# Optimization experiments

Measured on AMD Instinct MI355X. Metric: run time of the kernel, lower is better.

## Reference

```python
import jax, jax.numpy as jnp
import numpy as np

N = 50000      # nodes
E = 800000     # edges (avg degree 16)
G = 256        # graphs in batch
DIN = 126      # input feature dim (hardcoded in module)
H = 128        # dim_h


def _lin_init(key, fan_in, shape):
    s = 1.0 / np.sqrt(fan_in)
    return jax.random.uniform(key, shape, minval=-s, maxval=s, dtype=jnp.float32)


def setup_inputs() -> dict:
    key = jax.random.key(0)
    ks = iter(jax.random.split(key, 64))
    inp = {}
    inp["x"] = jax.random.normal(next(ks), (N, DIN), dtype=jnp.float32)
    inp["edge_attr"] = jax.random.normal(next(ks), (E, 4), dtype=jnp.float32)  # unused by the conv (edge_dim=None)
    dims = [(DIN, H), (H, H), (H, H)]
    for l, (i, o) in enumerate(dims, start=1):
        for nm, bnm in [("Wk", "bk"), ("Wq", "bq"), ("Wv", "bv"), ("Ws", "bs")]:
            inp[f"{nm}{l}"] = _lin_init(next(ks), i, (i, o))
            inp[f"{bnm}{l}"] = _lin_init(next(ks), i, (o,))
    inp["W4"] = _lin_init(next(ks), H, (H, 64))
    inp["b4"] = _lin_init(next(ks), H, (64,))
    inp["W5"] = _lin_init(next(ks), 64, (64, 1))
    inp["b5"] = _lin_init(next(ks), 64, (1,))
    inp["edge_index"] = jax.random.randint(next(ks), (2, E), 0, N, dtype=jnp.int64)
    inp["batch"] = jnp.sort(jax.random.randint(next(ks), (N,), 0, G, dtype=jnp.int64))
    return inp


def _res_gated_conv(x, src, dst, Wk, bk, Wq, bq, Wv, bv, Ws, bs):
    # PyG ResGatedGraphConv: out_i = skip(x_i) + sum_j sigmoid(K_i + Q_j) * V_j
    K = x @ Wk + bk   # [N, H] keys (destination / x_i)
    Q = x @ Wq + bq   # [N, H] queries (source / x_j)
    V = x @ Wv + bv   # [N, H] values (source / x_j)
    gate = jax.nn.sigmoid(K[dst] + Q[src])           # [E, H]
    msg = gate * V[src]                              # [E, H]
    agg = jax.ops.segment_sum(msg, dst, num_segments=x.shape[0])  # scatter-add to dst
    return agg + x @ Ws + bs  # lin_skip (no bias) + conv bias


def reference(x, edge_attr,
              Wk1, bk1, Wq1, bq1, Wv1, bv1, Ws1, bs1,
              Wk2, bk2, Wq2, bq2, Wv2, bv2, Ws2, bs2,
              Wk3, bk3, Wq3, bq3, Wv3, bv3, Ws3, bs3,
              W4, b4, W5, b5, edge_index, batch):
    src, dst = edge_index[0], edge_index[1]
    h = jax.nn.relu(_res_gated_conv(x, src, dst, Wk1, bk1, Wq1, bq1, Wv1, bv1, Ws1, bs1))
    h = jax.nn.relu(_res_gated_conv(h, src, dst, Wk2, bk2, Wq2, bq2, Wv2, bv2, Ws2, bs2))
    h = _res_gated_conv(h, src, dst, Wk3, bk3, Wq3, bq3, Wv3, bv3, Ws3, bs3)
    # global_add_pool over graphs
    hg = jax.ops.segment_sum(h, batch, num_segments=G)  # [G, H]
    hg = jax.nn.relu(hg @ W4 + b4)
    return jax.nn.sigmoid(hg @ W5 + b5)  # [G, 1]
```

## Files before the change

kernel.cpp:

```cpp
#include <hip/hip_runtime.h>

#define N_NODES 50000
#define N_EDGES 800000
#define N_GRAPHS 256
#define DIN 126
#define H 128
#define MP 50048
#define NBKT 196
#define NBA 100
#define CHA 8000

typedef __attribute__((ext_vector_type(8))) _Float16 half8v;
typedef __attribute__((ext_vector_type(4))) _Float16 half4v;
typedef __attribute__((ext_vector_type(4))) float f32x4;
typedef __attribute__((ext_vector_type(2))) float f32x2;

__global__ __launch_bounds__(256) void conv_A(const float* __restrict__ X, int M, int Kd,
                                              _Float16* __restrict__ A16)
{
    const int t = blockIdx.x * 256 + threadIdx.x;
    const int row = t >> 4;
    if (row >= MP) return;
    const int k0 = (t & 15) * 8;
    half8v v8;
    #pragma unroll
    for (int j = 0; j < 8; ++j) {
        const int k = k0 + j;
        float v = 0.f;
        if (row < M && k < Kd) v = X[(size_t)row * Kd + k];
        v8[j] = (_Float16)v;
    }
    *(half8v*)&A16[(size_t)row * 128 + k0] = v8;
}

struct WPtrs { const float* w[12]; };

__global__ __launch_bounds__(256) void conv_W3(WPtrs P, _Float16* __restrict__ Wt16)
{
    const int t = blockIdx.x * 256 + threadIdx.x;
    if (t >= 3 * 512 * 128) return;
    const int layer = t >> 16;
    const int r = t & 65535;
    const int n = r >> 7, k = r & 127;
    const int mtx = n >> 7, cc = n & 127;
    const int Kd = (layer == 0) ? DIN : H;
    const float* W = P.w[layer * 4 + mtx];
    const float v = (k < Kd) ? W[(size_t)k * 128 + cc] : 0.f;
    Wt16[t] = (_Float16)v;
}

__device__ __forceinline__ void dense_out512(const uint2 (&ldsO)[64][32],
                                             unsigned char* __restrict__ dst,
                                             int row0, int M, int t)
{
    #pragma unroll
    for (int i = 0; i < 2; ++i) {
        const int idx = i * 512 + t;
        const int rr = idx >> 4, c16 = idx & 15;
        const int ch = c16 ^ ((rr & 15) >> 1);
        const uint2 a = ldsO[rr][2 * ch];
        const uint2 b = ldsO[rr][2 * ch + 1];
        if (row0 + rr < M) {
            uint4 o;
            if (rr & 1) { o.x = b.x; o.y = b.y; o.z = a.x; o.w = a.y; }
            else        { o.x = a.x; o.y = a.y; o.z = b.x; o.w = b.y; }
            *(uint4*)(dst + (size_t)(row0 + rr) * 256 + c16 * 16) = o;
        }
    }
}

__device__ __forceinline__ void compute_acc16(const _Float16 (&ldsA)[2][64 * 64],
                                              const _Float16* __restrict__ Wt16,
                                              int mtx, int fr, int kq, int colbase,
                                              f32x4 (&acc)[4])
{
    #pragma unroll
    for (int step = 0; step < 4; ++step) {
        const int kg = step * 4 + kq;
        const int kh = kg >> 3, kk = kg & 7;
        half8v a[4];
        #pragma unroll
        for (int m = 0; m < 4; ++m) {
            const int ar = m * 16 + fr;
            const int slot = kk ^ (ar & 7);
            a[m] = *(const half8v*)&ldsA[kh][ar * 64 + slot * 8];
        }
        const size_t wo = (size_t)(mtx * 128 + colbase + fr) * 128 + kg * 8;
        const half8v w = *(const half8v*)&Wt16[wo];
        #pragma unroll
        for (int m = 0; m < 4; ++m)
            acc[m] = __builtin_amdgcn_mfma_f32_16x16x32_f16(w, a[m], acc[m], 0, 0, 0);
    }
}

__global__ __launch_bounds__(512) void gemm_mfma(
    const _Float16* __restrict__ A16, const _Float16* __restrict__ Wt16,
    const float* __restrict__ bias0, const float* __restrict__ bias1,
    const float* __restrict__ bias2, const float* __restrict__ bias3,
    _Float16* __restrict__ OEK, unsigned char* __restrict__ QV8,
    _Float16* __restrict__ OS, int M)
{
    __shared__ _Float16 ldsA[2][64 * 64];
    __shared__ uint2 ldsO[64][32];
    const int t = threadIdx.x;
    const int l = t & 63, w = t >> 6;
    const int row0 = blockIdx.x * 64;
    const int fr = l & 15;
    const int kq = l >> 4;
    const int colbase = w * 16;

    #pragma unroll
    for (int i = 0; i < 2; ++i) {
        const int gi = i * 512 + t;
        const int kh = gi >> 9;
        const int r = (gi >> 3) & 63;
        const int j = gi & 7;
        const int slot = j ^ (r & 7);
        *(half8v*)&ldsA[kh][r * 64 + slot * 8] =
            *(const half8v*)&A16[(size_t)(row0 + r) * 128 + kh * 64 + j * 8];
    }
    __syncthreads();

    const int c0 = colbase + kq * 4;
    const int qd = (c0 >> 2) ^ fr;

    {
        f32x4 acc[4] = {};
        compute_acc16(ldsA, Wt16, 0, fr, kq, colbase, acc);
        const float4 bv = *(const float4*)&bias0[c0];
        #pragma unroll
        for (int m = 0; m < 4; ++m) {
            const int rl = m * 16 + fr;
            half4v o;
            o[0] = (_Float16)__expf(-(acc[m][0] + bv.x));
            o[1] = (_Float16)__expf(-(acc[m][1] + bv.y));
            o[2] = (_Float16)__expf(-(acc[m][2] + bv.z));
            o[3] = (_Float16)__expf(-(acc[m][3] + bv.w));
            ldsO[rl][qd] = *(uint2*)&o;
        }
    }
    __syncthreads();
    dense_out512(ldsO, (unsigned char*)OEK, row0, M, t);
    __syncthreads();

    {
        f32x4 acc[4] = {};
        compute_acc16(ldsA, Wt16, 1, fr, kq, colbase, acc);
        const float4 bv = *(const float4*)&bias1[c0];
        #pragma unroll
        for (int m = 0; m < 4; ++m) {
            const int rl = m * 16 + fr;
            const float e0 = __expf(-(acc[m][0] + bv.x));
            const float e1 = __expf(-(acc[m][1] + bv.y));
            const float e2 = __expf(-(acc[m][2] + bv.z));
            const float e3 = __expf(-(acc[m][3] + bv.w));
            int p = 0;
            p = __builtin_amdgcn_cvt_pk_fp8_f32(e0, e1, p, false);
            p = __builtin_amdgcn_cvt_pk_fp8_f32(e2, e3, p, true);
            ((unsigned*)&ldsO[rl][qd])[0] = (unsigned)p;
        }
    }
    {
        f32x4 acc[4] = {};
        compute_acc16(ldsA, Wt16, 2, fr, kq, colbase, acc);
        const float4 bv = *(const float4*)&bias2[c0];
        #pragma unroll
        for (int m = 0; m < 4; ++m) {
            const int rl = m * 16 + fr;
            int p = 0;
            p = __builtin_amdgcn_cvt_pk_fp8_f32(acc[m][0] + bv.x,
                                                acc[m][1] + bv.y, p, false);
            p = __builtin_amdgcn_cvt_pk_fp8_f32(acc[m][2] + bv.z,
                                                acc[m][3] + bv.w, p, true);
            ((unsigned*)&ldsO[rl][qd])[1] = (unsigned)p;
        }
    }
    __syncthreads();
    dense_out512(ldsO, QV8, row0, M, t);
    __syncthreads();

    {
        f32x4 acc[4] = {};
        compute_acc16(ldsA, Wt16, 3, fr, kq, colbase, acc);
        const float4 bv = *(const float4*)&bias3[c0];
        #pragma unroll
        for (int m = 0; m < 4; ++m) {
            const int rl = m * 16 + fr;
            half4v o;
            o[0] = (_Float16)(acc[m][0] + bv.x);
            o[1] = (_Float16)(acc[m][1] + bv.y);
            o[2] = (_Float16)(acc[m][2] + bv.z);
            o[3] = (_Float16)(acc[m][3] + bv.w);
            ldsO[rl][qd] = *(uint2*)&o;
        }
    }
    __syncthreads();
    dense_out512(ldsO, (unsigned char*)OS, row0, M, t);
}

__global__ __launch_bounds__(256) void pA_hist(const int* __restrict__ ei,
                                               int* __restrict__ ghA)
{
    __shared__ int lh[NBKT];
    const int t = threadIdx.x, b = blockIdx.x;
    if (t < NBKT) lh[t] = 0;
    __syncthreads();
    const int e0 = b * CHA;
    for (int i = t; i < CHA; i += 256)
        atomicAdd(&lh[ei[N_EDGES + e0 + i] >> 8], 1);
    __syncthreads();
    if (t < NBKT) ghA[t * NBA + b] = lh[t];
}

__global__ __launch_bounds__(1024) void pA_scan(int* __restrict__ g)
{
    __shared__ int part[1024];
    const int t = threadIdx.x;
    const int NT = NBKT * NBA;
    const int CH = 20;
    const int base = t * CH;
    int s = 0;
    for (int i = 0; i < CH; ++i) {
        const int idx = base + i;
        if (idx < NT) s += g[idx];
    }
    part[t] = s;
    __syncthreads();
    for (int d = 1; d < 1024; d <<= 1) {
        const int v = (t >= d) ? part[t - d] : 0;
        __syncthreads();
        part[t] += v;
        __syncthreads();
    }
    int run = (t == 0) ? 0 : part[t - 1];
    for (int i = 0; i < CH; ++i) {
        const int idx = base + i;
        if (idx < NT) { const int c = g[idx]; g[idx] = run; run += c; }
    }
    if (t == 1023) g[NT] = part[1023];
}

__global__ __launch_bounds__(256) void pA_scat(const int* __restrict__ ei,
                                               const int* __restrict__ gbase,
                                               unsigned int* __restrict__ ebuf)
{
    __shared__ int cur[NBKT];
    const int t = threadIdx.x, b = blockIdx.x;
    if (t < NBKT) cur[t] = gbase[t * NBA + b];
    __syncthreads();
    const int e0 = b * CHA;
    for (int i = t; i < CHA; i += 256) {
        const unsigned d = (unsigned)ei[N_EDGES + e0 + i];
        const unsigned s = (unsigned)ei[e0 + i];
        const int pos = atomicAdd(&cur[d >> 8], 1);
        ebuf[pos] = (d << 16) | s;
    }
}

__global__ __launch_bounds__(256) void pB_build(const unsigned int* __restrict__ ebuf,
                                                const int* __restrict__ gbase,
                                                int* __restrict__ off,
                                                int* __restrict__ csr)
{
    __shared__ int lh[256], sc[256];
    const int t = threadIdx.x, b = blockIdx.x;
    const int beg = gbase[b * NBA];
    const int end = gbase[(b + 1) * NBA];
    lh[t] = 0;
    __syncthreads();
    for (int i = beg + t; i < end; i += 256)
        atomicAdd(&lh[(ebuf[i] >> 16) & 255], 1);
    __syncthreads();
    const int c = lh[t];
    sc[t] = c;
    __syncthreads();
    for (int d = 1; d < 256; d <<= 1) {
        const int v = (t >= d) ? sc[t - d] : 0;
        __syncthreads();
        sc[t] += v;
        __syncthreads();
    }
    const int excl = sc[t] - c;
    const int nd = b * 256 + t;
    if (nd <= N_NODES) off[nd] = beg + excl;
    __syncthreads();
    lh[t] = beg + excl;
    __syncthreads();
    for (int i = beg + t; i < end; i += 256) {
        const unsigned p = ebuf[i];
        const int pos = atomicAdd(&lh[(p >> 16) & 255], 1);
        csr[pos] = (int)(p & 0xFFFFu);
    }
}

template<int FUSE>
__global__ __launch_bounds__(256) void agg_csr(
    const _Float16* __restrict__ EKb, const unsigned char* __restrict__ QV8,
    const int* __restrict__ off, const int* __restrict__ csr_src,
    _Float16* __restrict__ hSkip, _Float16* __restrict__ A16, int Nn)
{
    const int node = blockIdx.x * 4 + (threadIdx.x >> 6);
    if (node >= Nn) return;
    const int lane = threadIdx.x & 63;
    const int grp = lane >> 4;
    const int sub = lane & 15;
    const int q = sub * 8;

    const half8v ek8 = *(const half8v*)(EKb + (size_t)node * H + q);
    float ek[8];
    #pragma unroll
    for (int i = 0; i < 8; ++i) ek[i] = (float)ek8[i];
    float acc[8] = {};

    const int begin = off[node], end = off[node + 1];
    for (int j0 = begin; j0 < end; j0 += 64) {
        const int nrem = end - j0;
        const int nk = nrem < 64 ? nrem : 64;
        const int sv = (lane < nk) ? csr_src[j0 + lane] : 0;
        #pragma unroll 4
        for (int k = 0; k < nk; k += 4) {
            const int myk = k + grp;
            const int s = __shfl(sv, myk < nk ? myk : 0);
            if (myk < nk) {
                const uint4 p = *(const uint4*)(QV8 + (size_t)s * 256 + sub * 16);
                const f32x2 ea = __builtin_amdgcn_cvt_pk_f32_fp8(p.x, false);
                const f32x2 eb = __builtin_amdgcn_cvt_pk_f32_fp8(p.x, true);
                const f32x2 va = __builtin_amdgcn_cvt_pk_f32_fp8(p.y, false);
                const f32x2 vb = __builtin_amdgcn_cvt_pk_f32_fp8(p.y, true);
                const f32x2 ec = __builtin_amdgcn_cvt_pk_f32_fp8(p.z, false);
                const f32x2 ed = __builtin_amdgcn_cvt_pk_f32_fp8(p.z, true);
                const f32x2 vc = __builtin_amdgcn_cvt_pk_f32_fp8(p.w, false);
                const f32x2 vd = __builtin_amdgcn_cvt_pk_f32_fp8(p.w, true);
                acc[0] = fmaf(va[0], __builtin_amdgcn_rcpf(fmaf(ek[0], ea[0], 1.f)), acc[0]);
                acc[1] = fmaf(va[1], __builtin_amdgcn_rcpf(fmaf(ek[1], ea[1], 1.f)), acc[1]);
                acc[2] = fmaf(vb[0], __builtin_amdgcn_rcpf(fmaf(ek[2], eb[0], 1.f)), acc[2]);
                acc[3] = fmaf(vb[1], __builtin_amdgcn_rcpf(fmaf(ek[3], eb[1], 1.f)), acc[3]);
                acc[4] = fmaf(vc[0], __builtin_amdgcn_rcpf(fmaf(ek[4], ec[0], 1.f)), acc[4]);
                acc[5] = fmaf(vc[1], __builtin_amdgcn_rcpf(fmaf(ek[5], ec[1], 1.f)), acc[5]);
                acc[6] = fmaf(vd[0], __builtin_amdgcn_rcpf(fmaf(ek[6], ed[0], 1.f)), acc[6]);
                acc[7] = fmaf(vd[1], __builtin_amdgcn_rcpf(fmaf(ek[7], ed[1], 1.f)), acc[7]);
            }
        }
    }
    #pragma unroll
    for (int i = 0; i < 8; ++i) {
        acc[i] += __shfl_xor(acc[i], 16);
        acc[i] += __shfl_xor(acc[i], 32);
    }
    if (grp == 0) {
        const half8v sk8 = *(const half8v*)(hSkip + (size_t)node * H + q);
        half8v hv;
        if (FUSE) {
            #pragma unroll
            for (int j = 0; j < 8; ++j)
                hv[j] = (_Float16)fmaxf((float)sk8[j] + acc[j], 0.f);
            *(half8v*)&A16[(size_t)node * 128 + q] = hv;
        } else {
            #pragma unroll
            for (int j = 0; j < 8; ++j)
                hv[j] = (_Float16)((float)sk8[j] + acc[j]);
            *(half8v*)&hSkip[(size_t)node * H + q] = hv;
        }
    }
}

__global__ __launch_bounds__(256) void gstart_kernel(const int* __restrict__ batch,
                                                     int* __restrict__ gstart, int Nn)
{
    const int n = blockIdx.x * 256 + threadIdx.x;
    if (n >= Nn) return;
    const int b = batch[n];
    const int bp = (n == 0) ? -1 : batch[n - 1];
    for (int g = bp + 1; g <= b; ++g) gstart[g] = n;
    if (n == Nn - 1)
        for (int g = b + 1; g <= N_GRAPHS; ++g) gstart[g] = Nn;
}

__global__ __launch_bounds__(128) void pool_seg(const _Float16* __restrict__ h,
                                                const int* __restrict__ gstart,
                                                float* __restrict__ hg)
{
    const int g = blockIdx.x;
    const int part = blockIdx.y;
    const int t = threadIdx.x;
    const int b0 = gstart[g], b1 = gstart[g + 1];
    float acc = 0.f;
    for (int n = b0 + part; n < b1; n += 4) acc += (float)h[(size_t)n * H + t];
    atomicAdd(&hg[(size_t)g * H + t], acc);
}

__global__ __launch_bounds__(64) void mlp_kernel(
    const float* __restrict__ hg,
    const float* __restrict__ W4, const float* __restrict__ b4,
    const float* __restrict__ W5, const float* __restrict__ b5,
    float* __restrict__ out)
{
    const int g = blockIdx.x;
    const int c = threadIdx.x;
    __shared__ float hrow[H];
    for (int k = c; k < H; k += 64) hrow[k] = hg[(size_t)g * H + k];
    __syncthreads();
    float s = b4[c];
    #pragma unroll 8
    for (int k = 0; k < H; ++k) s += hrow[k] * W4[(size_t)k * 64 + c];
    s = fmaxf(s, 0.f) * W5[c];
    #pragma unroll
    for (int off = 32; off > 0; off >>= 1) s += __shfl_down(s, off);
    if (c == 0) out[g] = 1.f / (1.f + __expf(-(s + b5[0])));
}

extern "C" void kernel_launch(void* const* d_in, const int* in_sizes, int n_in,
                              void* d_out, int out_size, void* d_ws, size_t ws_size,
                              hipStream_t stream)
{
    const float* x = (const float*)d_in[0];
    const float *Wk[3], *bk[3], *Wq[3], *bq[3], *Wv[3], *bv[3], *Wsk[3], *bs[3];
    for (int l = 0; l < 3; ++l) {
        const int base = 2 + l * 8;
        Wk[l]  = (const float*)d_in[base + 0]; bk[l] = (const float*)d_in[base + 1];
        Wq[l]  = (const float*)d_in[base + 2]; bq[l] = (const float*)d_in[base + 3];
        Wv[l]  = (const float*)d_in[base + 4]; bv[l] = (const float*)d_in[base + 5];
        Wsk[l] = (const float*)d_in[base + 6]; bs[l] = (const float*)d_in[base + 7];
    }
    const float* W4 = (const float*)d_in[26];
    const float* b4 = (const float*)d_in[27];
    const float* W5 = (const float*)d_in[28];
    const float* b5 = (const float*)d_in[29];
    const int* ei    = (const int*)d_in[30];
    const int* batch = (const int*)d_in[31];
    float* out = (float*)d_out;

    const size_t NH = (size_t)N_NODES * H;
    const size_t AH = (size_t)MP * 128;
    const size_t WH3 = (size_t)3 * 512 * 128;
    _Float16*      EKb  = (_Float16*)d_ws;
    _Float16*      hbuf = EKb + NH;
    unsigned char* QV8  = (unsigned char*)(hbuf + NH);
    _Float16*      A16  = (_Float16*)(QV8 + 2 * NH);
    _Float16*      Wt16 = A16 + AH;
    float*         hg   = (float*)(Wt16 + WH3);
    int*           off  = (int*)(hg + (size_t)N_GRAPHS * H);
    int*           csr  = off + (N_NODES + 1);
    unsigned int*  ebuf = (unsigned int*)(csr + N_EDGES);
    int*           ghA  = (int*)(ebuf + N_EDGES);
    int*           gst  = ghA + (NBKT * NBA + 1);
    const size_t need = (size_t)N_GRAPHS * H * sizeof(float)
                      + 2 * NH * sizeof(unsigned char)
                      + (2 * NH + AH + WH3) * sizeof(_Float16)
                      + (size_t)(N_NODES + 1 + 2 * N_EDGES + NBKT * NBA + 1
                                 + N_GRAPHS + 1) * sizeof(int);
    if (ws_size < need) return;

    const int ablk = (N_NODES + 3) / 4;
    const int nblk = (N_NODES + 255) / 256;
    const int cablk = (MP * 16) / 256;
    const int ggrid = MP / 64;
    const dim3 pgrid(N_GRAPHS, 4);

    hipMemsetAsync(hg, 0, (size_t)N_GRAPHS * H * sizeof(float), stream);

    pA_hist<<<NBA, 256, 0, stream>>>(ei, ghA);
    pA_scan<<<1, 1024, 0, stream>>>(ghA);
    pA_scat<<<NBA, 256, 0, stream>>>(ei, ghA, ebuf);
    pB_build<<<NBKT, 256, 0, stream>>>(ebuf, ghA, off, csr);
    gstart_kernel<<<nblk, 256, 0, stream>>>(batch, gst, N_NODES);
    WPtrs wp;
    for (int l = 0; l < 3; ++l) {
        wp.w[l * 4 + 0] = Wk[l];
        wp.w[l * 4 + 1] = Wq[l];
        wp.w[l * 4 + 2] = Wv[l];
        wp.w[l * 4 + 3] = Wsk[l];
    }
    conv_W3<<<768, 256, 0, stream>>>(wp, Wt16);

    conv_A<<<cablk, 256, 0, stream>>>(x, N_NODES, DIN, A16);
    gemm_mfma<<<ggrid, 512, 0, stream>>>(A16, Wt16,
        bk[0], bq[0], bv[0], bs[0], EKb, QV8, hbuf, N_NODES);
    agg_csr<1><<<ablk, 256, 0, stream>>>(EKb, QV8, off, csr, hbuf, A16, N_NODES);

    gemm_mfma<<<ggrid, 512, 0, stream>>>(A16, Wt16 + 512 * 128,
        bk[1], bq[1], bv[1], bs[1], EKb, QV8, hbuf, N_NODES);
    agg_csr<1><<<ablk, 256, 0, stream>>>(EKb, QV8, off, csr, hbuf, A16, N_NODES);

    gemm_mfma<<<ggrid, 512, 0, stream>>>(A16, Wt16 + 1024 * 128,
        bk[2], bq[2], bv[2], bs[2], EKb, QV8, hbuf, N_NODES);
    agg_csr<0><<<ablk, 256, 0, stream>>>(EKb, QV8, off, csr, hbuf, A16, N_NODES);

    pool_seg<<<pgrid, 128, 0, stream>>>(hbuf, gst, hg);
    mlp_kernel<<<N_GRAPHS, 64, 0, stream>>>(hg, W4, b4, W5, b5, out);
}
```

Before: 296.9 us.

## Parallelize bucket offset scan across blocks and merge weight/input conversion kernels

Replaces the single-block 1024-thread scan of the bucket histogram with a three-phase multi-block scan (block reduce, scan of block sums, per-block scan with offsets). It also fuses the weight transpose/convert and input fp16 conversion into one launch. The goal is to cut serial single-block scan latency and one kernel launch, at the cost of two extra small launches for the scan.

```diff
diff --git a/kernel.cpp b/kernel.cpp
--- a/kernel.cpp
+++ b/kernel.cpp
@@ -9,44 +9,44 @@
 #define NBKT 196
 #define NBA 100
 #define CHA 8000
+#define NSC 77
 
 typedef __attribute__((ext_vector_type(8))) _Float16 half8v;
 typedef __attribute__((ext_vector_type(4))) _Float16 half4v;
 typedef __attribute__((ext_vector_type(4))) float f32x4;
 typedef __attribute__((ext_vector_type(2))) float f32x2;
 
-__global__ __launch_bounds__(256) void conv_A(const float* __restrict__ X, int M, int Kd,
-                                              _Float16* __restrict__ A16)
-{
-    const int t = blockIdx.x * 256 + threadIdx.x;
-    const int row = t >> 4;
-    if (row >= MP) return;
-    const int k0 = (t & 15) * 8;
-    half8v v8;
-    #pragma unroll
-    for (int j = 0; j < 8; ++j) {
-        const int k = k0 + j;
-        float v = 0.f;
-        if (row < M && k < Kd) v = X[(size_t)row * Kd + k];
-        v8[j] = (_Float16)v;
-    }
-    *(half8v*)&A16[(size_t)row * 128 + k0] = v8;
-}
-
 struct WPtrs { const float* w[12]; };
 
-__global__ __launch_bounds__(256) void conv_W3(WPtrs P, _Float16* __restrict__ Wt16)
-{
-    const int t = blockIdx.x * 256 + threadIdx.x;
-    if (t >= 3 * 512 * 128) return;
-    const int layer = t >> 16;
-    const int r = t & 65535;
-    const int n = r >> 7, k = r & 127;
-    const int mtx = n >> 7, cc = n & 127;
-    const int Kd = (layer == 0) ? DIN : H;
-    const float* W = P.w[layer * 4 + mtx];
-    const float v = (k < Kd) ? W[(size_t)k * 128 + cc] : 0.f;
-    Wt16[t] = (_Float16)v;
+__global__ __launch_bounds__(256) void conv_prep(WPtrs P, const float* __restrict__ X,
+                                                 _Float16* __restrict__ Wt16,
+                                                 _Float16* __restrict__ A16)
+{
+    if (blockIdx.x < 768) {
+        const int t = blockIdx.x * 256 + threadIdx.x;
+        const int layer = t >> 16;
+        const int r = t & 65535;
+        const int n = r >> 7, k = r & 127;
+        const int mtx = n >> 7, cc = n & 127;
+        const int Kd = (layer == 0) ? DIN : H;
+        const float* W = P.w[layer * 4 + mtx];
+        const float v = (k < Kd) ? W[(size_t)k * 128 + cc] : 0.f;
+        Wt16[t] = (_Float16)v;
+    } else {
+        const int t = (blockIdx.x - 768) * 256 + threadIdx.x;
+        const int row = t >> 4;
+        if (row >= MP) return;
+        const int k0 = (t & 15) * 8;
+        half8v v8;
+        #pragma unroll
+        for (int j = 0; j < 8; ++j) {
+            const int k = k0 + j;
+            float v = 0.f;
+            if (row < N_NODES && k < DIN) v = X[(size_t)row * DIN + k];
+            v8[j] = (_Float16)v;
+        }
+        *(half8v*)&A16[(size_t)row * 128 + k0] = v8;
+    }
 }
 
 __device__ __forceinline__ void dense_out512(const uint2 (&ldsO)[64][32],
@@ -212,32 +212,70 @@
     if (t < NBKT) ghA[t * NBA + b] = lh[t];
 }
 
-__global__ __launch_bounds__(1024) void pA_scan(int* __restrict__ g)
-{
-    __shared__ int part[1024];
+__global__ __launch_bounds__(256) void sc_p1(const int* __restrict__ g,
+                                             int* __restrict__ bsum)
+{
+    __shared__ int red[256];
     const int t = threadIdx.x;
-    const int NT = NBKT * NBA;
-    const int CH = 20;
-    const int base = t * CH;
-    int s = 0;
-    for (int i = 0; i < CH; ++i) {
-        const int idx = base + i;
-        if (idx < NT) s += g[idx];
-    }
-    part[t] = s;
-    __syncthreads();
-    for (int d = 1; d < 1024; d <<= 1) {
-        const int v = (t >= d) ? part[t - d] : 0;
-        __syncthreads();
-        part[t] += v;
-        __syncthreads();
-    }
-    int run = (t == 0) ? 0 : part[t - 1];
-    for (int i = 0; i < CH; ++i) {
-        const int idx = base + i;
-        if (idx < NT) { const int c = g[idx]; g[idx] = run; run += c; }
-    }
-    if (t == 1023) g[NT] = part[1023];
+    const int i = blockIdx.x * 256 + t;
+    red[t] = (i < NBKT * NBA) ? g[i] : 0;
+    __syncthreads();
+    for (int d = 128; d > 0; d >>= 1) {
+        if (t < d) red[t] += red[t + d];
+        __syncthreads();
+    }
+    if (t == 0) bsum[blockIdx.x] = red[0];
+}
+
+__global__ __launch_bounds__(128) void sc_p2(const int* __restrict__ bsum,
+                                             int* __restrict__ bsoff,
+                                             int* __restrict__ g)
+{
+    __shared__ int sc[128];
+    const int t = threadIdx.x;
+    const int v = (t < NSC) ? bsum[t] : 0;
+    sc[t] = v;
+    __syncthreads();
+    #pragma unroll
+    for (int d = 1; d < 128; d <<= 1) {
+        const int a = (t >= d) ? sc[t - d] : 0;
+        __syncthreads();
+        sc[t] += a;
+        __syncthreads();
+    }
+    if (t < NSC) bsoff[t] = sc[t] - v;
+    if (t == 127) g[NBKT * NBA] = sc[127];
+}
+
+__global__ __launch_bounds__(256) void sc_p3(int* __restrict__ g,
+                                             const int* __restrict__ bsoff)
+{
+    __shared__ int sc[256];
+    const int t = threadIdx.x;
+    const int i = blockIdx.x * 256 + t;
+    const int v = (i < NBKT * NBA) ? g[i] : 0;
+    sc[t] = v;
+    __syncthreads();
+    #pragma unroll
+    for (int d = 1; d < 256; d <<= 1) {
+        const int a = (t >= d) ? sc[t - d] : 0;
+        __syncthreads();
+        sc[t] += a;
+        __syncthreads();
+    }
+    if (i < NBKT * NBA) g[i] = bsoff[blockIdx.x] + sc[t] - v;
+}
+
+__global__ __launch_bounds__(256) void gstart_kernel(const int* __restrict__ batch,
+                                                     int* __restrict__ gstart, int Nn)
+{
+    const int n = blockIdx.x * 256 + threadIdx.x;
+    if (n >= Nn) return;
+    const int b = batch[n];
+    const int bp = (n == 0) ? -1 : batch[n - 1];
+    for (int g = bp + 1; g <= b; ++g) gstart[g] = n;
+    if (n == Nn - 1)
+        for (int g = b + 1; g <= N_GRAPHS; ++g) gstart[g] = Nn;
 }
 
 __global__ __launch_bounds__(256) void pA_scat(const int* __restrict__ ei,
@@ -364,18 +402,6 @@
     }
 }
 
-__global__ __launch_bounds__(256) void gstart_kernel(const int* __restrict__ batch,
-                                                     int* __restrict__ gstart, int Nn)
-{
-    const int n = blockIdx.x * 256 + threadIdx.x;
-    if (n >= Nn) return;
-    const int b = batch[n];
-    const int bp = (n == 0) ? -1 : batch[n - 1];
-    for (int g = bp + 1; g <= b; ++g) gstart[g] = n;
-    if (n == Nn - 1)
-        for (int g = b + 1; g <= N_GRAPHS; ++g) gstart[g] = Nn;
-}
-
 __global__ __launch_bounds__(128) void pool_seg(const _Float16* __restrict__ h,
                                                 const int* __restrict__ gstart,
                                                 float* __restrict__ hg)
@@ -444,11 +470,13 @@
     unsigned int*  ebuf = (unsigned int*)(csr + N_EDGES);
     int*           ghA  = (int*)(ebuf + N_EDGES);
     int*           gst  = ghA + (NBKT * NBA + 1);
+    int*           bsum = gst + (N_GRAPHS + 1);
+    int*           bsoff= bsum + NSC;
     const size_t need = (size_t)N_GRAPHS * H * sizeof(float)
                       + 2 * NH * sizeof(unsigned char)
                       + (2 * NH + AH + WH3) * sizeof(_Float16)
                       + (size_t)(N_NODES + 1 + 2 * N_EDGES + NBKT * NBA + 1
-                                 + N_GRAPHS + 1) * sizeof(int);
+                                 + N_GRAPHS + 1 + 2 * NSC) * sizeof(int);
     if (ws_size < need) return;
 
     const int ablk = (N_NODES + 3) / 4;
@@ -460,7 +488,9 @@
     hipMemsetAsync(hg, 0, (size_t)N_GRAPHS * H * sizeof(float), stream);
 
     pA_hist<<<NBA, 256, 0, stream>>>(ei, ghA);
-    pA_scan<<<1, 1024, 0, stream>>>(ghA);
+    sc_p1<<<NSC, 256, 0, stream>>>(ghA, bsum);
+    sc_p2<<<1, 128, 0, stream>>>(bsum, bsoff, ghA);
+    sc_p3<<<NSC, 256, 0, stream>>>(ghA, bsoff);
     pA_scat<<<NBA, 256, 0, stream>>>(ei, ghA, ebuf);
     pB_build<<<NBKT, 256, 0, stream>>>(ebuf, ghA, off, csr);
     gstart_kernel<<<nblk, 256, 0, stream>>>(batch, gst, N_NODES);
@@ -471,9 +501,8 @@
         wp.w[l * 4 + 2] = Wv[l];
         wp.w[l * 4 + 3] = Wsk[l];
     }
-    conv_W3<<<768, 256, 0, stream>>>(wp, Wt16);
-
-    conv_A<<<cablk, 256, 0, stream>>>(x, N_NODES, DIN, A16);
+    conv_prep<<<768 + cablk, 256, 0, stream>>>(wp, x, Wt16, A16);
+
     gemm_mfma<<<ggrid, 512, 0, stream>>>(A16, Wt16,
         bk[0], bq[0], bv[0], bs[0], EKb, QV8, hbuf, N_NODES);
     agg_csr<1><<<ablk, 256, 0, stream>>>(EKb, QV8, off, csr, hbuf, A16, N_NODES);
```

Result: faster. 272.7 us (-8.1%).
